# Optimization experiments

Measured on AMD Instinct MI355X. Metric: run time of the kernel, lower is better.

## Reference

```python
import jax, jax.numpy as jnp
import numpy as np

B, S, D, H, Dh, F, L, V = 16, 512, 512, 8, 64, 2048, 6, 32000


def _layer_norm(x, g, b):
    m = x.mean(-1, keepdims=True)
    v = ((x - m) ** 2).mean(-1, keepdims=True)
    return (x - m) / jnp.sqrt(v + 1e-5) * g + b


def setup_inputs() -> dict:
    key = jax.random.key(0)
    ks = jax.random.split(key, 18)
    s = 0.02
    x = jax.random.randint(ks[0], (B, S), 0, V)
    batch_length = jax.random.randint(ks[1], (B,), 0, S)
    embed = (jax.random.normal(ks[2], (V, D)) * s).at[0].set(0.0)  # padding_idx=0 row zeroed
    Wq = jax.random.normal(ks[3], (L, D, H * Dh)) * s
    Wk = jax.random.normal(ks[4], (L, D, H * Dh)) * s
    Wv = jax.random.normal(ks[5], (L, D, H * Dh)) * s
    Wo = jax.random.normal(ks[6], (L, H * Dh, D)) * s
    bo = jnp.zeros((L, D))
    ln1_g = jnp.ones((L, D)); ln1_b = jnp.zeros((L, D))
    W1 = jax.random.normal(ks[7], (L, D, F)) * s
    b1 = jnp.zeros((L, F))
    W2 = jax.random.normal(ks[8], (L, F, D)) * s
    b2 = jnp.zeros((L, D))
    ln2_g = jnp.ones((L, D)); ln2_b = jnp.zeros((L, D))
    return dict(x=x, batch_length=batch_length, embed=embed, Wq=Wq, Wk=Wk, Wv=Wv,
                Wo=Wo, bo=bo, ln1_g=ln1_g, ln1_b=ln1_b, W1=W1, b1=b1, W2=W2,
                b2=b2, ln2_g=ln2_g, ln2_b=ln2_b)


def reference(x, batch_length, embed, Wq, Wk, Wv, Wo, bo, ln1_g, ln1_b,
              W1, b1, W2, b2, ln2_g, ln2_b):
    # sinusoidal positional encoding, exact replication (2.0*i/d with full index i)
    pos = jnp.arange(S, dtype=jnp.float32)[:, None]
    i = jnp.arange(D, dtype=jnp.float32)[None, :]
    ang = pos / jnp.power(10000.0, 2.0 * i / D)
    pe = ang.at[:, 0::2].set(jnp.sin(ang[:, 0::2])).at[:, 1::2].set(jnp.cos(ang[:, 1::2]))
    # per-sample PE truncated at batch_length (rest zero)
    len_mask = (jnp.arange(S)[None, :] < batch_length[:, None]).astype(pe.dtype)
    h = embed[x] + pe[None, :, :] * len_mask[:, :, None]  # [B,S,D]
    # padding mask: True where token==0, expanded to [B,S,S]; torch repeat(H,1,1) -> heads major
    pad = (x == 0)
    pmask = jnp.broadcast_to(pad[:, None, :], (B, S, S))
    mrep = jnp.tile(pmask, (H, 1, 1))  # [H*B, S, S], faithful to torch .repeat
    scale = 1.0 / np.sqrt(Dh).astype(np.float32)
    for l in range(L):
        # faithful .view(B*H, -1, Dh) on [B,S,H*Dh] contiguous memory
        q = (h @ Wq[l]).reshape(B * H, S, Dh)
        k = (h @ Wk[l]).reshape(B * H, S, Dh)
        v = (h @ Wv[l]).reshape(B * H, S, Dh)
        att = jnp.einsum('bqd,bkd->bqk', q, k) * scale  # [B*H,S,S]
        att = jnp.where(mrep, -1e9, att)
        att = jax.nn.softmax(att, axis=2)
        ctx = (att @ v).reshape(B, S, H * Dh)
        o = ctx @ Wo[l] + bo[l]
        h = _layer_norm(h + o, ln1_g[l], ln1_b[l])
        f = jax.nn.relu(h @ W1[l] + b1[l]) @ W2[l] + b2[l]
        h = _layer_norm(h + f, ln2_g[l], ln2_b[l])
    return h
```

## Files before the change

kernel.cpp:

```cpp
#include <hip/hip_runtime.h>
#include <hip/hip_bf16.h>
#include <cmath>

#define B_  16
#define S_  512
#define D_  512
#define F_  2048
#define L_  6
#define MT  8192

typedef __attribute__((ext_vector_type(8))) __bf16 bf16x8;
typedef __attribute__((ext_vector_type(4))) float  f32x4;

__device__ __forceinline__ unsigned short f2bf(float f) {
  return __builtin_bit_cast(unsigned short, __float2bfloat16(f));
}

__device__ __forceinline__ void gload16(const void* g, void* l) {
  __builtin_amdgcn_global_load_lds(
      (const __attribute__((address_space(1))) void*)g,
      (__attribute__((address_space(3))) void*)l, 16, 0, 0);
}

__global__ void embed_pe_kernel(const int* __restrict__ x,
                                const int* __restrict__ blen,
                                const float* __restrict__ emb,
                                float* __restrict__ h,
                                unsigned short* __restrict__ hbf) {
  int bs = blockIdx.x;
  int b = bs >> 9, s = bs & 511;
  int tok = x[bs];
  bool pe = s < blen[b];
  const float* er = emb + (long)tok * D_;
  long rb = (long)bs * D_;
  for (int d = threadIdx.x; d < D_; d += 256) {
    float e = er[d];
    if (pe) {
      float ex = (2.0f * (float)d) / 512.0f;
      float ang = (float)s / powf(10000.0f, ex);
      e += (d & 1) ? cosf(ang) : sinf(ang);
    }
    h[rb + d] = e;
    hbf[rb + d] = f2bf(e);
  }
}

__global__ void mask_build_kernel(const int* __restrict__ x,
                                  unsigned int* __restrict__ mw) {
  int t = threadIdx.x;
  int b = t >> 4, wd = t & 15;
  unsigned int m = 0;
  for (int j = 0; j < 32; j++)
    if (x[b * 512 + wd * 32 + j] == 0) m |= (1u << j);
  mw[b * 16 + wd] = m;
}

__global__ __launch_bounds__(256)
void wconv_kernel(const float* __restrict__ in, unsigned short* __restrict__ out,
                  int K, int N, long inls, long outls) {
  __shared__ float tile[32][33];
  const float* ip = in + (long)blockIdx.z * inls;
  unsigned short* op = out + (long)blockIdx.z * outls;
  int k0 = blockIdx.y * 32, n0 = blockIdx.x * 32;
  int tx = threadIdx.x & 31, ty = threadIdx.x >> 5;
  for (int i = ty; i < 32; i += 8) tile[i][tx] = ip[(long)(k0 + i) * N + n0 + tx];
  __syncthreads();
  for (int i = ty; i < 32; i += 8) op[(long)(n0 + i) * K + k0 + tx] = f2bf(tile[tx][i]);
}

template<int BMv, int MINW>
__global__ __launch_bounds__(256, MINW)
void gemm_bf16(const unsigned short* __restrict__ A,
               const unsigned short* __restrict__ Bt,
               const float* __restrict__ bias,
               float* __restrict__ C, unsigned short* __restrict__ Cbf,
               int M, int N, int K, int relu, int qkv) {
  constexpr int MFR = 4;
  constexpr int NFR = (BMv == 128) ? 4 : 2;
  __shared__ unsigned short Al[2][BMv * 32];
  __shared__ unsigned short Bl[2][128 * 32];
  int t = threadIdx.x;
  int lane = t & 63, wid = t >> 6;

  int flat = blockIdx.y * gridDim.x + blockIdx.x;
  int npx = (gridDim.x * gridDim.y) >> 3;
  int w = (flat & 7) * npx + (flat >> 3);
  int bx = w % gridDim.x, by = w / gridDim.x;

  int rbase = by * BMv, cbase = bx * 128;
  int wr = (BMv == 128) ? (wid >> 1) * 64 : 0;
  int wc = (BMv == 128) ? (wid & 1) * 64 : wid * 32;

  f32x4 acc[MFR][NFR];
#pragma unroll
  for (int i = 0; i < MFR; i++)
#pragma unroll
    for (int j = 0; j < NFR; j++) acc[i][j] = (f32x4){0.f, 0.f, 0.f, 0.f};

  int srow = t >> 2;
  int sc = (((t & 3) ^ ((t >> 3) & 3)) << 3);
  const unsigned short* Ag  = A  + (long)(rbase + srow) * K + sc;
  const unsigned short* Ag2 = A  + (long)(rbase + 64 + srow) * K + sc;
  const unsigned short* Bg  = Bt + (long)(cbase + srow) * K + sc;
  const unsigned short* Bg2 = Bt + (long)(cbase + 64 + srow) * K + sc;

  auto stage = [&](int bi, int kt) {
    gload16(Ag + kt, &Al[bi][t * 8]);
    if constexpr (BMv == 128) gload16(Ag2 + kt, &Al[bi][2048 + t * 8]);
    gload16(Bg + kt, &Bl[bi][t * 8]);
    gload16(Bg2 + kt, &Bl[bi][2048 + t * 8]);
  };

  int fr = lane & 15;
  int c4 = lane >> 4;

  int nt = K >> 5;
  stage(0, 0);
  int cur = 0;
  for (int tt = 0; tt < nt; ++tt) {
    if (tt + 1 < nt) {
      stage(cur ^ 1, (tt + 1) << 5);
      if constexpr (BMv == 128)
        asm volatile("s_waitcnt vmcnt(4)" ::: "memory");
      else
        asm volatile("s_waitcnt vmcnt(3)" ::: "memory");
    } else {
      asm volatile("s_waitcnt vmcnt(0)" ::: "memory");
    }
    __builtin_amdgcn_s_barrier();

    bf16x8 a[MFR], b[NFR];
#pragma unroll
    for (int m = 0; m < MFR; m++) {
      int R = wr + m * 16 + fr;
      a[m] = *(const bf16x8*)&Al[cur][R * 32 + ((c4 ^ ((R >> 1) & 3)) << 3)];
    }
#pragma unroll
    for (int n = 0; n < NFR; n++) {
      int R = wc + n * 16 + fr;
      b[n] = *(const bf16x8*)&Bl[cur][R * 32 + ((c4 ^ ((R >> 1) & 3)) << 3)];
    }
#pragma unroll
    for (int m = 0; m < MFR; m++)
#pragma unroll
      for (int n = 0; n < NFR; n++)
        acc[m][n] = __builtin_amdgcn_mfma_f32_16x16x32_bf16(a[m], b[n], acc[m][n], 0, 0, 0);
    __builtin_amdgcn_s_barrier();
    cur ^= 1;
  }

  if (BMv == 128 && qkv) {
#pragma unroll
    for (int m = 0; m < MFR; m++) {
#pragma unroll
      for (int n = 0; n < NFR; n++) {
        int col = cbase + wc + n * 16 + fr;
#pragma unroll
        for (int j = 0; j < 4; j++) {
          long row = rbase + wr + m * 16 + (lane >> 4) * 4 + j;
          unsigned short v = f2bf(acc[m][n][j]);
          if (col < 1024) {
            Cbf[(col < 512 ? 0L : 4194304L - 512L) + row * 512 + col] = v;
          } else {
            int cc = col - 1024;
            Cbf[8388608L + (row >> 6) * 32768 + (long)(cc & 63) * 512 +
                ((row & 63) << 3) + (cc >> 6)] = v;
          }
        }
      }
    }
  } else {
#pragma unroll
    for (int m = 0; m < MFR; m++) {
#pragma unroll
      for (int n = 0; n < NFR; n++) {
        int col = cbase + wc + n * 16 + fr;
        float bv = bias ? bias[col] : 0.0f;
#pragma unroll
        for (int j = 0; j < 4; j++) {
          long row = rbase + wr + m * 16 + (lane >> 4) * 4 + j;
          float v = acc[m][n][j] + bv;
          if (relu) v = fmaxf(v, 0.0f);
          if (C)   C[row * N + col] = v;
          if (Cbf) Cbf[row * N + col] = f2bf(v);
        }
      }
    }
  }
}

__global__ __launch_bounds__(256, 3)
void attn_mfma(const unsigned short* __restrict__ qbf,
               const unsigned short* __restrict__ kbf,
               const unsigned short* __restrict__ vtbf,
               const unsigned int* __restrict__ maskw,
               unsigned short* __restrict__ ctxbf) {
  __shared__ unsigned short sb[2][8192];
  int t = threadIdx.x;
  int lane = t & 63, w = t >> 6;
  int c = lane & 15, h = lane >> 4;

  int flat = blockIdx.y * 8 + blockIdx.x;
  int wk = (flat & 7) * 128 + (flat >> 3);
  int qt = wk & 7, bh = wk >> 3;

  long bhb = (long)bh << 15;
  int mb = bh & 15;

  unsigned int mwa[16];
#pragma unroll
  for (int i = 0; i < 16; i++)
    mwa[i] = (unsigned int)__builtin_amdgcn_readfirstlane((int)maskw[mb * 16 + i]);

  const bf16x8* qp = (const bf16x8*)(qbf + bhb + (long)(qt * 64 + w * 16 + c) * 64);
  bf16x8 qf0 = qp[h], qf1 = qp[h + 4];

  auto stageK = [&](int bi, int ch) {
#pragma unroll
    for (int i = 0; i < 4; i++) {
      int idx = t + 256 * i;
      int kr = idx >> 3, g = idx & 7;
      gload16(kbf + bhb + (long)(ch * 128 + kr) * 64 + ((g ^ (kr & 7)) << 3),
              &sb[bi][idx * 8]);
    }
  };
  auto stageV = [&](int bi, int ch) {
#pragma unroll
    for (int i = 0; i < 4; i++) {
      int idx = t + 256 * i;
      int d = idx >> 4, g = idx & 15;
      gload16(vtbf + bhb + (long)d * 512 + ch * 128 + ((g ^ (d & 15)) << 3),
              &sb[bi][idx * 8]);
    }
  };

  f32x4 acc[32];
#pragma unroll
  for (int F = 0; F < 32; F++) acc[F] = (f32x4){0.f, 0.f, 0.f, 0.f};

  stageK(0, 0);
  int cur = 0;
#pragma unroll
  for (int ch = 0; ch < 4; ch++) {
    if (ch < 3) stageK(cur ^ 1, ch + 1);
    else        stageV(cur ^ 1, 0);
    asm volatile("s_waitcnt vmcnt(4)" ::: "memory");
    __builtin_amdgcn_s_barrier();
#pragma unroll
    for (int f = 0; f < 8; f++) {
      int R = f * 16 + c;
      int ro = R * 64;
      bf16x8 a0 = *(const bf16x8*)&sb[cur][ro + ((h ^ (R & 7)) << 3)];
      bf16x8 a1 = *(const bf16x8*)&sb[cur][ro + (((h + 4) ^ (R & 7)) << 3)];
      acc[ch * 8 + f] = __builtin_amdgcn_mfma_f32_16x16x32_bf16(a0, qf0, acc[ch * 8 + f], 0, 0, 0);
      acc[ch * 8 + f] = __builtin_amdgcn_mfma_f32_16x16x32_bf16(a1, qf1, acc[ch * 8 + f], 0, 0, 0);
    }
    __builtin_amdgcn_s_barrier();
    cur ^= 1;
  }

#pragma unroll
  for (int F = 0; F < 32; F++) {
    unsigned int nib = (mwa[F >> 1] >> (((F & 1) << 4) + (h << 2))) & 0xFu;
#pragma unroll
    for (int j = 0; j < 4; j++)
      acc[F][j] = (nib & (1u << j)) ? -1e9f : acc[F][j] * 0.125f;
  }

  float mx = -3.0e38f;
#pragma unroll
  for (int F = 0; F < 32; F++)
#pragma unroll
    for (int j = 0; j < 4; j++) mx = fmaxf(mx, acc[F][j]);
  mx = fmaxf(mx, __shfl_xor(mx, 16));
  mx = fmaxf(mx, __shfl_xor(mx, 32));

  float sm = 0.f;
  unsigned int pk[64];
#pragma unroll
  for (int F = 0; F < 32; F++) {
    float e0 = __expf(acc[F][0] - mx); sm += e0;
    float e1 = __expf(acc[F][1] - mx); sm += e1;
    float e2 = __expf(acc[F][2] - mx); sm += e2;
    float e3 = __expf(acc[F][3] - mx); sm += e3;
    pk[2 * F]     = (unsigned int)f2bf(e0) | ((unsigned int)f2bf(e1) << 16);
    pk[2 * F + 1] = (unsigned int)f2bf(e2) | ((unsigned int)f2bf(e3) << 16);
  }
  sm += __shfl_xor(sm, 16);
  sm += __shfl_xor(sm, 32);

  float rs0 = 1.0f / __shfl(sm, h * 4 + 0);
  float rs1 = 1.0f / __shfl(sm, h * 4 + 1);
  float rs2 = 1.0f / __shfl(sm, h * 4 + 2);
  float rs3 = 1.0f / __shfl(sm, h * 4 + 3);

  f32x4 o[4];
#pragma unroll
  for (int n = 0; n < 4; n++) o[n] = (f32x4){0.f, 0.f, 0.f, 0.f};
  int l0 = c | ((lane & 16) << 1);
  int l1 = l0 + 16;
  bool hb = (lane & 32) != 0;

#pragma unroll
  for (int ch = 0; ch < 4; ch++) {
    if (ch < 3) {
      stageV(cur ^ 1, ch + 1);
      asm volatile("s_waitcnt vmcnt(4)" ::: "memory");
    } else {
      asm volatile("s_waitcnt vmcnt(0)" ::: "memory");
    }
    __builtin_amdgcn_s_barrier();
#pragma unroll
    for (int sub = 0; sub < 4; sub++) {
      int kt4 = (ch * 4 + sub) * 4;
      unsigned int a0 = __shfl((int)pk[kt4],     l0);
      unsigned int a1 = __shfl((int)pk[kt4 + 1], l0);
      unsigned int a2 = __shfl((int)pk[kt4],     l1);
      unsigned int a3 = __shfl((int)pk[kt4 + 1], l1);
      unsigned int b0 = __shfl((int)pk[kt4 + 2], l0);
      unsigned int b1 = __shfl((int)pk[kt4 + 3], l0);
      unsigned int b2 = __shfl((int)pk[kt4 + 2], l1);
      unsigned int b3 = __shfl((int)pk[kt4 + 3], l1);
      uint4 aw;
      aw.x = hb ? b0 : a0; aw.y = hb ? b1 : a1;
      aw.z = hb ? b2 : a2; aw.w = hb ? b3 : a3;
      bf16x8 af = __builtin_bit_cast(bf16x8, aw);
#pragma unroll
      for (int n = 0; n < 4; n++) {
        int dl = n * 16 + c;
        bf16x8 vf = *(const bf16x8*)&sb[cur][dl * 128 + (((sub * 4 + h) ^ (dl & 15)) << 3)];
        o[n] = __builtin_amdgcn_mfma_f32_16x16x32_bf16(af, vf, o[n], 0, 0, 0);
      }
    }
    __builtin_amdgcn_s_barrier();
    cur ^= 1;
  }

  unsigned short* cp = ctxbf + bhb + (long)(qt * 64 + w * 16) * 64;
#pragma unroll
  for (int n = 0; n < 4; n++) {
    cp[(h * 4 + 0) * 64 + n * 16 + c] = f2bf(o[n][0] * rs0);
    cp[(h * 4 + 1) * 64 + n * 16 + c] = f2bf(o[n][1] * rs1);
    cp[(h * 4 + 2) * 64 + n * 16 + c] = f2bf(o[n][2] * rs2);
    cp[(h * 4 + 3) * 64 + n * 16 + c] = f2bf(o[n][3] * rs3);
  }
}

__global__ __launch_bounds__(256)
void ln_kernel(const float* __restrict__ a, const float* __restrict__ r,
               const float* __restrict__ g, const float* __restrict__ be,
               float* __restrict__ out, unsigned short* __restrict__ outbf) {
  int w = threadIdx.x >> 6, lane = threadIdx.x & 63;
  long row = (long)blockIdx.x * 4 + w;
  long base = row * D_ + lane * 8;
  float4 a0 = *(const float4*)(a + base);
  float4 a1 = *(const float4*)(a + base + 4);
  float4 r0 = *(const float4*)(r + base);
  float4 r1 = *(const float4*)(r + base + 4);
  float xv[8] = {a0.x + r0.x, a0.y + r0.y, a0.z + r0.z, a0.w + r0.w,
                 a1.x + r1.x, a1.y + r1.y, a1.z + r1.z, a1.w + r1.w};
  float s = 0;
#pragma unroll
  for (int e = 0; e < 8; e++) s += xv[e];
#pragma unroll
  for (int off = 1; off < 64; off <<= 1) s += __shfl_xor(s, off);
  float m = s * (1.0f / 512.0f);
  float vs = 0;
#pragma unroll
  for (int e = 0; e < 8; e++) { float d = xv[e] - m; vs += d * d; }
#pragma unroll
  for (int off = 1; off < 64; off <<= 1) vs += __shfl_xor(vs, off);
  float rstd = 1.0f / sqrtf(vs * (1.0f / 512.0f) + 1e-5f);
  int gb = lane * 8;
  float o[8];
#pragma unroll
  for (int e = 0; e < 8; e++) o[e] = (xv[e] - m) * rstd * g[gb + e] + be[gb + e];
  *(float4*)(out + base)     = make_float4(o[0], o[1], o[2], o[3]);
  *(float4*)(out + base + 4) = make_float4(o[4], o[5], o[6], o[7]);
  ushort4 u0, u1;
  u0.x = f2bf(o[0]); u0.y = f2bf(o[1]); u0.z = f2bf(o[2]); u0.w = f2bf(o[3]);
  u1.x = f2bf(o[4]); u1.y = f2bf(o[5]); u1.z = f2bf(o[6]); u1.w = f2bf(o[7]);
  *(ushort4*)(outbf + base)     = u0;
  *(ushort4*)(outbf + base + 4) = u1;
}

extern "C" void kernel_launch(void* const* d_in, const int* in_sizes, int n_in,
                              void* d_out, int out_size, void* d_ws, size_t ws_size,
                              hipStream_t stream) {
  const int*   x    = (const int*)d_in[0];
  const int*   blen = (const int*)d_in[1];
  const float* emb  = (const float*)d_in[2];
  const float* Wq   = (const float*)d_in[3];
  const float* Wk   = (const float*)d_in[4];
  const float* Wv   = (const float*)d_in[5];
  const float* Wo   = (const float*)d_in[6];
  const float* bo   = (const float*)d_in[7];
  const float* ln1g = (const float*)d_in[8];
  const float* ln1b = (const float*)d_in[9];
  const float* W1   = (const float*)d_in[10];
  const float* b1   = (const float*)d_in[11];
  const float* W2   = (const float*)d_in[12];
  const float* b2   = (const float*)d_in[13];
  const float* ln2g = (const float*)d_in[14];
  const float* ln2b = (const float*)d_in[15];
  float* out = (float*)d_out;

  float* ws_f = (float*)d_ws;
  const long M4 = 4194304L;
  float* h   = ws_f;
  float* tmp = ws_f + M4;
  unsigned short* U = (unsigned short*)(ws_f + 2 * M4);
  unsigned short* h_bf   = U;
  unsigned short* q_bf   = U + M4;
  unsigned short* k_bf   = U + 2 * M4;
  unsigned short* vt_bf  = U + 3 * M4;
  unsigned short* ctx_bf = U + 4 * M4;
  unsigned short* mid_bf = q_bf;
  unsigned short* Wqkvt  = U + 5 * M4;
  unsigned short* Wot    = Wqkvt + 6L * 1536 * 512;
  unsigned short* W1t    = Wot   + 6L * 512 * 512;
  unsigned short* W2t    = W1t   + 6L * 2048 * 512;
  unsigned int*   maskw  = (unsigned int*)(W2t + 6L * 512 * 2048);

  wconv_kernel<<<dim3(16, 16, 6), 256, 0, stream>>>(Wq, Wqkvt,            512, 512,  262144L, 786432L);
  wconv_kernel<<<dim3(16, 16, 6), 256, 0, stream>>>(Wk, Wqkvt + 262144,   512, 512,  262144L, 786432L);
  wconv_kernel<<<dim3(16, 16, 6), 256, 0, stream>>>(Wv, Wqkvt + 524288,   512, 512,  262144L, 786432L);
  wconv_kernel<<<dim3(16, 16, 6), 256, 0, stream>>>(Wo, Wot,              512, 512,  262144L, 262144L);
  wconv_kernel<<<dim3(64, 16, 6), 256, 0, stream>>>(W1, W1t,              512, 2048, 1048576L, 1048576L);
  wconv_kernel<<<dim3(16, 64, 6), 256, 0, stream>>>(W2, W2t,              2048, 512, 1048576L, 1048576L);
  mask_build_kernel<<<1, 256, 0, stream>>>(x, maskw);
  embed_pe_kernel<<<MT, 256, 0, stream>>>(x, blen, emb, h, h_bf);

  dim3 gqkv(12, 64), g2048(16, 64), g512b(4, 128), gattn(8, 128);

  for (int l = 0; l < L_; l++) {
    const unsigned short* wqkv = Wqkvt + (long)l * 1536 * 512;
    const unsigned short* wo   = Wot   + (long)l * 512 * 512;
    const unsigned short* w1   = W1t   + (long)l * 2048 * 512;
    const unsigned short* w2   = W2t   + (long)l * 512 * 2048;

    gemm_bf16<128, 2><<<gqkv, 256, 0, stream>>>(h_bf, wqkv, nullptr, nullptr, q_bf,
                                                MT, 1536, 512, 0, 1);
    attn_mfma<<<gattn, 256, 0, stream>>>(q_bf, k_bf, vt_bf, maskw, ctx_bf);
    gemm_bf16<64, 3><<<g512b, 256, 0, stream>>>(ctx_bf, wo, bo + (long)l * D_, tmp, nullptr,
                                                MT, 512, 512, 0, 0);
    ln_kernel<<<MT / 4, 256, 0, stream>>>(h, tmp, ln1g + (long)l * D_,
                                          ln1b + (long)l * D_, h, h_bf);
    gemm_bf16<128, 2><<<g2048, 256, 0, stream>>>(h_bf, w1, b1 + (long)l * F_, nullptr, mid_bf,
                                                 MT, 2048, 512, 1, 0);
    gemm_bf16<64, 3><<<g512b, 256, 0, stream>>>(mid_bf, w2, b2 + (long)l * D_, tmp, nullptr,
                                                MT, 512, 2048, 0, 0);
    ln_kernel<<<MT / 4, 256, 0, stream>>>(h, tmp, ln2g + (long)l * D_,
                                          ln2b + (long)l * D_,
                                          (l == L_ - 1) ? out : h, h_bf);
  }
}
```

Measured before the change: 972.9 us.

## Triple-buffer LDS staging in GEMM and attention kernels for deeper prefetch

Moves the GEMM and attention kernels from double-buffered to triple-buffered LDS, so each loop iteration issues loads two tiles ahead and waits on correspondingly larger vmcnt thresholds. The attention kernel's K/V chunk rotation is rewritten to fit three buffers, and the QKV GEMM launch bound is raised to three waves per SIMD. The aim is to hide more global-load latency behind MFMA work. The cost is 50% more shared memory per block, which may lower occupancy, and the attention buffer indexing and wait counts must stay exactly right for correctness.

Result: slower. 1.021 ms (+5.0%).

```diff
diff --git a/kernel.cpp b/kernel.cpp
--- a/kernel.cpp
+++ b/kernel.cpp
@@ -77,8 +77,8 @@
                int M, int N, int K, int relu, int qkv) {
   constexpr int MFR = 4;
   constexpr int NFR = (BMv == 128) ? 4 : 2;
-  __shared__ unsigned short Al[2][BMv * 32];
-  __shared__ unsigned short Bl[2][128 * 32];
+  __shared__ unsigned short Al[3][BMv * 32];
+  __shared__ unsigned short Bl[3][128 * 32];
   int t = threadIdx.x;
   int lane = t & 63, wid = t >> 6;
 
@@ -116,10 +116,17 @@
 
   int nt = K >> 5;
   stage(0, 0);
+  stage(1, 32);
   int cur = 0;
   for (int tt = 0; tt < nt; ++tt) {
-    if (tt + 1 < nt) {
-      stage(cur ^ 1, (tt + 1) << 5);
+    if (tt + 2 < nt) {
+      int s2 = cur + 2; if (s2 >= 3) s2 -= 3;
+      stage(s2, (tt + 2) << 5);
+      if constexpr (BMv == 128)
+        asm volatile("s_waitcnt vmcnt(8)" ::: "memory");
+      else
+        asm volatile("s_waitcnt vmcnt(6)" ::: "memory");
+    } else if (tt + 1 < nt) {
       if constexpr (BMv == 128)
         asm volatile("s_waitcnt vmcnt(4)" ::: "memory");
       else
@@ -146,7 +153,7 @@
       for (int n = 0; n < NFR; n++)
         acc[m][n] = __builtin_amdgcn_mfma_f32_16x16x32_bf16(a[m], b[n], acc[m][n], 0, 0, 0);
     __builtin_amdgcn_s_barrier();
-    cur ^= 1;
+    cur = (cur + 1 == 3) ? 0 : cur + 1;
   }
 
   if (BMv == 128 && qkv) {
@@ -195,7 +202,7 @@
                const unsigned short* __restrict__ vtbf,
                const unsigned int* __restrict__ maskw,
                unsigned short* __restrict__ ctxbf) {
-  __shared__ unsigned short sb[2][8192];
+  __shared__ unsigned short sb[3][8192];
   int t = threadIdx.x;
   int lane = t & 63, w = t >> 6;
   int c = lane & 15, h = lane >> 4;
@@ -239,24 +246,24 @@
   for (int F = 0; F < 32; F++) acc[F] = (f32x4){0.f, 0.f, 0.f, 0.f};
 
   stageK(0, 0);
-  int cur = 0;
+  stageK(1, 1);
 #pragma unroll
   for (int ch = 0; ch < 4; ch++) {
-    if (ch < 3) stageK(cur ^ 1, ch + 1);
-    else        stageV(cur ^ 1, 0);
-    asm volatile("s_waitcnt vmcnt(4)" ::: "memory");
-    __builtin_amdgcn_s_barrier();
+    if (ch < 2) stageK((ch + 2) % 3, ch + 2);
+    else        stageV((ch + 2) % 3, ch - 2);
+    asm volatile("s_waitcnt vmcnt(8)" ::: "memory");
+    __builtin_amdgcn_s_barrier();
+    const unsigned short* kb = sb[ch % 3];
 #pragma unroll
     for (int f = 0; f < 8; f++) {
       int R = f * 16 + c;
       int ro = R * 64;
-      bf16x8 a0 = *(const bf16x8*)&sb[cur][ro + ((h ^ (R & 7)) << 3)];
-      bf16x8 a1 = *(const bf16x8*)&sb[cur][ro + (((h + 4) ^ (R & 7)) << 3)];
+      bf16x8 a0 = *(const bf16x8*)&kb[ro + ((h ^ (R & 7)) << 3)];
+      bf16x8 a1 = *(const bf16x8*)&kb[ro + (((h + 4) ^ (R & 7)) << 3)];
       acc[ch * 8 + f] = __builtin_amdgcn_mfma_f32_16x16x32_bf16(a0, qf0, acc[ch * 8 + f], 0, 0, 0);
       acc[ch * 8 + f] = __builtin_amdgcn_mfma_f32_16x16x32_bf16(a1, qf1, acc[ch * 8 + f], 0, 0, 0);
     }
     __builtin_amdgcn_s_barrier();
-    cur ^= 1;
   }
 
 #pragma unroll
@@ -303,13 +310,16 @@
 
 #pragma unroll
   for (int ch = 0; ch < 4; ch++) {
-    if (ch < 3) {
-      stageV(cur ^ 1, ch + 1);
+    if (ch < 2) {
+      stageV(ch % 3, ch + 2);
+      asm volatile("s_waitcnt vmcnt(8)" ::: "memory");
+    } else if (ch == 2) {
       asm volatile("s_waitcnt vmcnt(4)" ::: "memory");
     } else {
       asm volatile("s_waitcnt vmcnt(0)" ::: "memory");
     }
     __builtin_amdgcn_s_barrier();
+    const unsigned short* vbuf = sb[(ch + 1) % 3];
 #pragma unroll
     for (int sub = 0; sub < 4; sub++) {
       int kt4 = (ch * 4 + sub) * 4;
@@ -328,12 +338,11 @@
 #pragma unroll
       for (int n = 0; n < 4; n++) {
         int dl = n * 16 + c;
-        bf16x8 vf = *(const bf16x8*)&sb[cur][dl * 128 + (((sub * 4 + h) ^ (dl & 15)) << 3)];
+        bf16x8 vf = *(const bf16x8*)&vbuf[dl * 128 + (((sub * 4 + h) ^ (dl & 15)) << 3)];
         o[n] = __builtin_amdgcn_mfma_f32_16x16x32_bf16(af, vf, o[n], 0, 0, 0);
       }
     }
     __builtin_amdgcn_s_barrier();
-    cur ^= 1;
   }
 
   unsigned short* cp = ctxbf + bhb + (long)(qt * 64 + w * 16) * 64;
@@ -439,7 +448,7 @@
     const unsigned short* w1   = W1t   + (long)l * 2048 * 512;
     const unsigned short* w2   = W2t   + (long)l * 512 * 2048;
 
-    gemm_bf16<128, 2><<<gqkv, 256, 0, stream>>>(h_bf, wqkv, nullptr, nullptr, q_bf,
+    gemm_bf16<128, 3><<<gqkv, 256, 0, stream>>>(h_bf, wqkv, nullptr, nullptr, q_bf,
                                                 MT, 1536, 512, 0, 1);
     attn_mfma<<<gattn, 256, 0, stream>>>(q_bf, k_bf, vt_bf, maskw, ctx_bf);
     gemm_bf16<64, 3><<<g512b, 256, 0, stream>>>(ctx_bf, wo, bo + (long)l * D_, tmp, nullptr,
```

## Split attention keys across two wave groups with 512-thread blocks

Applied to the files above, without the earlier changes.

The attention kernel now runs 8 waves per block, each pair of wave groups handling half of the 512 keys for the same 16 query rows. Softmax max and sum are combined across the halves through shared memory, and the partial P·V outputs are reduced through LDS before writing. All four K chunks and all four V chunks are staged at once into a 4-slot buffer, replacing the double-buffer loop. This halves per-wave register pressure (acc and pk arrays) and doubles the wave count to raise occupancy and latency hiding. The cost is more LDS per block, extra barriers, and a cross-wave reduction.

Result: slower. 1.019 ms (+4.7%).

```diff
diff --git a/kernel.cpp b/kernel.cpp
--- a/kernel.cpp
+++ b/kernel.cpp
@@ -189,15 +189,17 @@
   }
 }
 
-__global__ __launch_bounds__(256, 3)
+__global__ __launch_bounds__(512, 4)
 void attn_mfma(const unsigned short* __restrict__ qbf,
                const unsigned short* __restrict__ kbf,
                const unsigned short* __restrict__ vtbf,
                const unsigned int* __restrict__ maskw,
                unsigned short* __restrict__ ctxbf) {
-  __shared__ unsigned short sb[2][8192];
+  __shared__ unsigned short sb[4][8192];
+  __shared__ float red[2][8][64];
   int t = threadIdx.x;
   int lane = t & 63, w = t >> 6;
+  int qg = w & 3, kh = w >> 2;
   int c = lane & 15, h = lane >> 4;
 
   int flat = blockIdx.y * 8 + blockIdx.x;
@@ -212,56 +214,58 @@
   for (int i = 0; i < 16; i++)
     mwa[i] = (unsigned int)__builtin_amdgcn_readfirstlane((int)maskw[mb * 16 + i]);
 
-  const bf16x8* qp = (const bf16x8*)(qbf + bhb + (long)(qt * 64 + w * 16 + c) * 64);
+  const bf16x8* qp = (const bf16x8*)(qbf + bhb + (long)(qt * 64 + qg * 16 + c) * 64);
   bf16x8 qf0 = qp[h], qf1 = qp[h + 4];
 
-  auto stageK = [&](int bi, int ch) {
-#pragma unroll
-    for (int i = 0; i < 4; i++) {
-      int idx = t + 256 * i;
+  auto stageK = [&](int gc) {
+#pragma unroll
+    for (int i = 0; i < 2; i++) {
+      int idx = t + 512 * i;
       int kr = idx >> 3, g = idx & 7;
-      gload16(kbf + bhb + (long)(ch * 128 + kr) * 64 + ((g ^ (kr & 7)) << 3),
-              &sb[bi][idx * 8]);
+      gload16(kbf + bhb + (long)(gc * 128 + kr) * 64 + ((g ^ (kr & 7)) << 3),
+              &sb[gc][idx * 8]);
     }
   };
-  auto stageV = [&](int bi, int ch) {
-#pragma unroll
-    for (int i = 0; i < 4; i++) {
-      int idx = t + 256 * i;
+  auto stageV = [&](int gc) {
+#pragma unroll
+    for (int i = 0; i < 2; i++) {
+      int idx = t + 512 * i;
       int d = idx >> 4, g = idx & 15;
-      gload16(vtbf + bhb + (long)d * 512 + ch * 128 + ((g ^ (d & 15)) << 3),
-              &sb[bi][idx * 8]);
+      gload16(vtbf + bhb + (long)d * 512 + gc * 128 + ((g ^ (d & 15)) << 3),
+              &sb[gc][idx * 8]);
     }
   };
 
-  f32x4 acc[32];
-#pragma unroll
-  for (int F = 0; F < 32; F++) acc[F] = (f32x4){0.f, 0.f, 0.f, 0.f};
-
-  stageK(0, 0);
-  int cur = 0;
-#pragma unroll
-  for (int ch = 0; ch < 4; ch++) {
-    if (ch < 3) stageK(cur ^ 1, ch + 1);
-    else        stageV(cur ^ 1, 0);
-    asm volatile("s_waitcnt vmcnt(4)" ::: "memory");
+  stageK(0); stageK(2); stageK(1); stageK(3);
+
+  f32x4 acc[16];
+#pragma unroll
+  for (int F = 0; F < 16; F++) acc[F] = (f32x4){0.f, 0.f, 0.f, 0.f};
+
+#pragma unroll
+  for (int lc = 0; lc < 2; lc++) {
+    if (lc == 0) asm volatile("s_waitcnt vmcnt(4)" ::: "memory");
+    else         asm volatile("s_waitcnt vmcnt(0)" ::: "memory");
     __builtin_amdgcn_s_barrier();
+    const unsigned short* kb = sb[kh * 2 + lc];
 #pragma unroll
     for (int f = 0; f < 8; f++) {
       int R = f * 16 + c;
       int ro = R * 64;
-      bf16x8 a0 = *(const bf16x8*)&sb[cur][ro + ((h ^ (R & 7)) << 3)];
-      bf16x8 a1 = *(const bf16x8*)&sb[cur][ro + (((h + 4) ^ (R & 7)) << 3)];
-      acc[ch * 8 + f] = __builtin_amdgcn_mfma_f32_16x16x32_bf16(a0, qf0, acc[ch * 8 + f], 0, 0, 0);
-      acc[ch * 8 + f] = __builtin_amdgcn_mfma_f32_16x16x32_bf16(a1, qf1, acc[ch * 8 + f], 0, 0, 0);
-    }
-    __builtin_amdgcn_s_barrier();
-    cur ^= 1;
-  }
-
-#pragma unroll
-  for (int F = 0; F < 32; F++) {
-    unsigned int nib = (mwa[F >> 1] >> (((F & 1) << 4) + (h << 2))) & 0xFu;
+      bf16x8 a0 = *(const bf16x8*)&kb[ro + ((h ^ (R & 7)) << 3)];
+      bf16x8 a1 = *(const bf16x8*)&kb[ro + (((h + 4) ^ (R & 7)) << 3)];
+      acc[lc * 8 + f] = __builtin_amdgcn_mfma_f32_16x16x32_bf16(a0, qf0, acc[lc * 8 + f], 0, 0, 0);
+      acc[lc * 8 + f] = __builtin_amdgcn_mfma_f32_16x16x32_bf16(a1, qf1, acc[lc * 8 + f], 0, 0, 0);
+    }
+  }
+  __builtin_amdgcn_s_barrier();
+
+  stageV(0); stageV(2); stageV(1); stageV(3);
+
+#pragma unroll
+  for (int F = 0; F < 16; F++) {
+    int gc = kh * 2 + (F >> 3), f = F & 7;
+    unsigned int nib = (mwa[gc * 4 + (f >> 1)] >> (((f & 1) << 4) + (h << 2))) & 0xFu;
 #pragma unroll
     for (int j = 0; j < 4; j++)
       acc[F][j] = (nib & (1u << j)) ? -1e9f : acc[F][j] * 0.125f;
@@ -269,16 +273,19 @@
 
   float mx = -3.0e38f;
 #pragma unroll
-  for (int F = 0; F < 32; F++)
+  for (int F = 0; F < 16; F++)
 #pragma unroll
     for (int j = 0; j < 4; j++) mx = fmaxf(mx, acc[F][j]);
   mx = fmaxf(mx, __shfl_xor(mx, 16));
   mx = fmaxf(mx, __shfl_xor(mx, 32));
+  red[0][w][lane] = mx;
+  __builtin_amdgcn_s_barrier();
+  mx = fmaxf(mx, red[0][w ^ 4][lane]);
 
   float sm = 0.f;
-  unsigned int pk[64];
-#pragma unroll
-  for (int F = 0; F < 32; F++) {
+  unsigned int pk[32];
+#pragma unroll
+  for (int F = 0; F < 16; F++) {
     float e0 = __expf(acc[F][0] - mx); sm += e0;
     float e1 = __expf(acc[F][1] - mx); sm += e1;
     float e2 = __expf(acc[F][2] - mx); sm += e2;
@@ -288,6 +295,9 @@
   }
   sm += __shfl_xor(sm, 16);
   sm += __shfl_xor(sm, 32);
+  red[1][w][lane] = sm;
+  __builtin_amdgcn_s_barrier();
+  sm += red[1][w ^ 4][lane];
 
   float rs0 = 1.0f / __shfl(sm, h * 4 + 0);
   float rs1 = 1.0f / __shfl(sm, h * 4 + 1);
@@ -302,17 +312,14 @@
   bool hb = (lane & 32) != 0;
 
 #pragma unroll
-  for (int ch = 0; ch < 4; ch++) {
-    if (ch < 3) {
-      stageV(cur ^ 1, ch + 1);
-      asm volatile("s_waitcnt vmcnt(4)" ::: "memory");
-    } else {
-      asm volatile("s_waitcnt vmcnt(0)" ::: "memory");
-    }
+  for (int lc = 0; lc < 2; lc++) {
+    if (lc == 0) asm volatile("s_waitcnt vmcnt(4)" ::: "memory");
+    else         asm volatile("s_waitcnt vmcnt(0)" ::: "memory");
     __builtin_amdgcn_s_barrier();
+    const unsigned short* vbuf = sb[kh * 2 + lc];
 #pragma unroll
     for (int sub = 0; sub < 4; sub++) {
-      int kt4 = (ch * 4 + sub) * 4;
+      int kt4 = (lc * 4 + sub) * 4;
       unsigned int a0 = __shfl((int)pk[kt4],     l0);
       unsigned int a1 = __shfl((int)pk[kt4 + 1], l0);
       unsigned int a2 = __shfl((int)pk[kt4],     l1);
@@ -328,21 +335,35 @@
 #pragma unroll
       for (int n = 0; n < 4; n++) {
         int dl = n * 16 + c;
-        bf16x8 vf = *(const bf16x8*)&sb[cur][dl * 128 + (((sub * 4 + h) ^ (dl & 15)) << 3)];
+        bf16x8 vf = *(const bf16x8*)&vbuf[dl * 128 + (((sub * 4 + h) ^ (dl & 15)) << 3)];
         o[n] = __builtin_amdgcn_mfma_f32_16x16x32_bf16(af, vf, o[n], 0, 0, 0);
       }
     }
-    __builtin_amdgcn_s_barrier();
-    cur ^= 1;
-  }
-
-  unsigned short* cp = ctxbf + bhb + (long)(qt * 64 + w * 16) * 64;
-#pragma unroll
-  for (int n = 0; n < 4; n++) {
-    cp[(h * 4 + 0) * 64 + n * 16 + c] = f2bf(o[n][0] * rs0);
-    cp[(h * 4 + 1) * 64 + n * 16 + c] = f2bf(o[n][1] * rs1);
-    cp[(h * 4 + 2) * 64 + n * 16 + c] = f2bf(o[n][2] * rs2);
-    cp[(h * 4 + 3) * 64 + n * 16 + c] = f2bf(o[n][3] * rs3);
+  }
+  __builtin_amdgcn_s_barrier();
+
+  float* osb = (float*)sb;
+  if (kh) {
+#pragma unroll
+    for (int n = 0; n < 4; n++)
+#pragma unroll
+      for (int j = 0; j < 4; j++)
+        osb[((w - 4) * 64 + lane) * 16 + n * 4 + j] = o[n][j];
+  }
+  __builtin_amdgcn_s_barrier();
+  if (!kh) {
+    unsigned short* cp = ctxbf + bhb + (long)(qt * 64 + qg * 16) * 64;
+#pragma unroll
+    for (int n = 0; n < 4; n++) {
+      float t0 = o[n][0] + osb[(w * 64 + lane) * 16 + n * 4 + 0];
+      float t1 = o[n][1] + osb[(w * 64 + lane) * 16 + n * 4 + 1];
+      float t2 = o[n][2] + osb[(w * 64 + lane) * 16 + n * 4 + 2];
+      float t3 = o[n][3] + osb[(w * 64 + lane) * 16 + n * 4 + 3];
+      cp[(h * 4 + 0) * 64 + n * 16 + c] = f2bf(t0 * rs0);
+      cp[(h * 4 + 1) * 64 + n * 16 + c] = f2bf(t1 * rs1);
+      cp[(h * 4 + 2) * 64 + n * 16 + c] = f2bf(t2 * rs2);
+      cp[(h * 4 + 3) * 64 + n * 16 + c] = f2bf(t3 * rs3);
+    }
   }
 }
 
@@ -441,7 +462,7 @@
 
     gemm_bf16<128, 2><<<gqkv, 256, 0, stream>>>(h_bf, wqkv, nullptr, nullptr, q_bf,
                                                 MT, 1536, 512, 0, 1);
-    attn_mfma<<<gattn, 256, 0, stream>>>(q_bf, k_bf, vt_bf, maskw, ctx_bf);
+    attn_mfma<<<gattn, 512, 0, stream>>>(q_bf, k_bf, vt_bf, maskw, ctx_bf);
     gemm_bf16<64, 3><<<g512b, 256, 0, stream>>>(ctx_bf, wo, bo + (long)l * D_, tmp, nullptr,
                                                 MT, 512, 512, 0, 0);
     ln_kernel<<<MT / 4, 256, 0, stream>>>(h, tmp, ln1g + (long)l * D_,
```
